# Optimization experiments

Hardware: AMD Instinct MI355X
Metric: run time of the kernel (lower is better)

Reference implementation:

```python
import jax, jax.numpy as jnp
import numpy as np

WINDOW = 5  # window_size from init
C_COARSE = 256
C_FINE = 128


def _gather_windows(fine_nchw, b, lin_idx, stride, pad, w, wc):
    """Extract [M, w*w, C] windows centered on coarse grid cells.

    Equivalent to F.unfold(kernel=w, stride=stride, padding=pad) followed by
    rearrange('n (c ww) l -> n l ww c') and fancy-indexing [b, lin_idx],
    but gathers only the matched windows.
    """
    x = jnp.pad(fine_nchw, ((0, 0), (0, 0), (pad, pad), (pad, pad)))
    x = jnp.transpose(x, (0, 2, 3, 1))  # [N, Hp, Wp, C]
    r = lin_idx // wc
    c = lin_idx % wc
    offs = jnp.arange(w)
    rows = r[:, None] * stride + offs  # [M, w] (start = r*stride - pad, +pad shift)
    cols = c[:, None] * stride + offs  # [M, w]
    patches = x[b[:, None, None], rows[:, :, None], cols[:, None, :]]  # [M, w, w, C]
    return patches.reshape(patches.shape[0], w * w, patches.shape[-1])


def setup_inputs() -> dict:
    key = jax.random.key(0)
    ks = jax.random.split(key, 10)
    N, Hc, Hf, M = 2, 60, 240, 3000
    inp = {
        "coarse_image_feature_1": jax.random.normal(ks[0], (N, Hc * Hc, C_COARSE), jnp.float32),
        "coarse_image_feature_2": jax.random.normal(ks[1], (N, Hc * Hc, C_COARSE), jnp.float32),
        "fine_image_feature_1": jax.random.normal(ks[2], (N, C_FINE, Hf, Hf), jnp.float32),
        "fine_image_feature_2": jax.random.normal(ks[3], (N, C_FINE, Hf, Hf), jnp.float32),
        "batch_indices": jax.random.randint(ks[4], (M,), 0, N),
        "row_indices": jax.random.randint(ks[5], (M,), 0, Hc * Hc),
        "column_indices": jax.random.randint(ks[6], (M,), 0, Hc * Hc),
        "fine_height_width": Hf,
        "coarse_height_width": Hc,
        # learned params (kaiming-normal-ish weights, zero biases)
        "W_dp": jax.random.normal(ks[7], (C_FINE, C_COARSE), jnp.float32) * np.sqrt(2.0 / C_FINE),
        "b_dp": jnp.zeros((C_FINE,), jnp.float32),
        "W_merge": jax.random.normal(ks[8], (C_FINE, 2 * C_FINE), jnp.float32) * np.sqrt(2.0 / C_FINE),
        "b_merge": jnp.zeros((C_FINE,), jnp.float32),
    }
    return inp


def reference(coarse_image_feature_1, coarse_image_feature_2,
              fine_image_feature_1, fine_image_feature_2,
              batch_indices, row_indices, column_indices,
              fine_height_width, coarse_height_width,
              W_dp, b_dp, W_merge, b_merge):
    stride = fine_height_width // coarse_height_width
    pad = WINDOW // 2
    M = batch_indices.shape[0]

    f1 = _gather_windows(fine_image_feature_1, batch_indices, row_indices,
                         stride, pad, WINDOW, coarse_height_width)       # [M, ww, Cf]
    f2 = _gather_windows(fine_image_feature_2, batch_indices, column_indices,
                         stride, pad, WINDOW, coarse_height_width)       # [M, ww, Cf]

    coarse = jnp.concatenate([
        coarse_image_feature_1[batch_indices, row_indices],
        coarse_image_feature_2[batch_indices, column_indices],
    ], axis=0)                                                           # [2M, Cc]
    coarse = coarse @ W_dp.T + b_dp                                      # [2M, Cf]

    fine = jnp.concatenate([f1, f2], axis=0)                             # [2M, ww, Cf]
    combined = jnp.concatenate(
        [fine, jnp.broadcast_to(coarse[:, None, :], fine.shape)], axis=-1)  # [2M, ww, 2Cf]
    merged = combined @ W_merge.T + b_merge                              # [2M, ww, Cf]
    return merged[:M], merged[M:]
```

## Files before the change

kernel.cpp:

```cpp
#include <hip/hip_runtime.h>

#define HF 240
#define HC 60
#define STRIDEF 4
#define PADW 2
#define WIN 5
#define CC 256
#define CF 128
#define NPOS 25
#define NPX (HF*HF)
#define MPB 16
#define PXT 64

typedef __bf16 bf16x8 __attribute__((ext_vector_type(8)));
typedef __bf16 bf16x4 __attribute__((ext_vector_type(4)));
typedef float  f32x4  __attribute__((ext_vector_type(4)));

__global__ void k_prep(const float* __restrict__ W_dp, const float* __restrict__ b_dp,
                       const float* __restrict__ W_merge, const float* __restrict__ b_merge,
                       __bf16* __restrict__ Wm1h, float* __restrict__ W_effT,
                       float* __restrict__ b_eff) {
    const int j = blockIdx.x;
    const int k = threadIdx.x;
    const float* wm2 = W_merge + (size_t)j * (2 * CF) + CF;

    float acc = 0.f, accb = 0.f;
    for (int q = 0; q < CF; ++q) {
        const float wq = wm2[q];
        acc  += wq * W_dp[(size_t)q * CC + k];
        accb += wq * b_dp[q];
    }
    W_effT[(size_t)k * CF + j] = acc;

    if (k < CF)
        Wm1h[(size_t)j * CF + k] = (__bf16)W_merge[(size_t)j * (2 * CF) + k];
    if (k == 0)
        b_eff[j] = accb + b_merge[j];
}

__global__ void k_coarse(const float* __restrict__ c1, const float* __restrict__ c2,
                         const int* __restrict__ bidx, const int* __restrict__ ridx,
                         const int* __restrict__ cidx, int M,
                         const float* __restrict__ W_effT, const float* __restrict__ b_eff,
                         float* __restrict__ c_all) {
    const int m0 = blockIdx.x * MPB;
    const int j  = threadIdx.x;
    const int twoM = 2 * M;
    __shared__ float v[MPB * CC];

    const int nm = (twoM - m0) < MPB ? (twoM - m0) : MPB;
    for (int mm = 0; mm < nm; ++mm) {
        int m = m0 + mm;
        const float* src;
        if (m < M) src = c1 + ((size_t)bidx[m] * (HC * HC) + ridx[m]) * CC;
        else       src = c2 + ((size_t)bidx[m - M] * (HC * HC) + cidx[m - M]) * CC;
        v[mm * CC + j]      = src[j];
        v[mm * CC + j + CF] = src[j + CF];
    }
    __syncthreads();

    float acc[MPB];
    const float be = b_eff[j];
    #pragma unroll
    for (int mm = 0; mm < MPB; ++mm) acc[mm] = be;

    for (int k = 0; k < CC; k += 4) {
        float w0 = W_effT[(k + 0) * CF + j];
        float w1 = W_effT[(k + 1) * CF + j];
        float w2 = W_effT[(k + 2) * CF + j];
        float w3 = W_effT[(k + 3) * CF + j];
        #pragma unroll
        for (int mm = 0; mm < MPB; ++mm) {
            const f32x4 vv = *(const f32x4*)&v[mm * CC + k];
            acc[mm] += w0 * vv.x + w1 * vv.y + w2 * vv.z + w3 * vv.w;
        }
    }
    for (int mm = 0; mm < nm; ++mm)
        c_all[(size_t)(m0 + mm) * CF + j] = acc[mm];
}

__global__ __launch_bounds__(256) void k_tgemm(
    const float* __restrict__ f1, const float* __restrict__ f2,
    const __bf16* __restrict__ Wm1h, __bf16* __restrict__ V) {

    const int slot = blockIdx.y;
    const float* src = (slot >= 2 ? f2 : f1) + (size_t)(slot & 1) * CF * NPX;
    const int px0 = blockIdx.x * PXT;
    const int t  = threadIdx.x;
    const int l  = t & 63;
    const int w  = t >> 6;
    const int lo16 = l & 15;
    const int hi   = l >> 4;

    __shared__ __bf16 patch[PXT * CF];

    bf16x8 bfrag[2][4];
    #pragma unroll
    for (int nt2 = 0; nt2 < 2; ++nt2) {
        const int j = w * 32 + nt2 * 16 + lo16;
        #pragma unroll
        for (int kt = 0; kt < 4; ++kt)
            bfrag[nt2][kt] = *reinterpret_cast<const bf16x8*>(Wm1h + (size_t)j * CF + kt * 32 + hi * 8);
    }

    const int pxl = 4 * lo16;
    const int sw  = lo16 << 3;
    #pragma unroll
    for (int q = 0; q < 8; ++q) {
        const int ch = w * 32 + q * 4 + hi;
        const f32x4 vv = *reinterpret_cast<const f32x4*>(src + (size_t)ch * NPX + px0 + pxl);
        const int chs = ch ^ sw;
        patch[(pxl + 0) * CF + chs] = (__bf16)vv.x;
        patch[(pxl + 1) * CF + chs] = (__bf16)vv.y;
        patch[(pxl + 2) * CF + chs] = (__bf16)vv.z;
        patch[(pxl + 3) * CF + chs] = (__bf16)vv.w;
    }
    __syncthreads();

    f32x4 acc[4][2];
    #pragma unroll
    for (int mt = 0; mt < 4; ++mt)
        #pragma unroll
        for (int nt2 = 0; nt2 < 2; ++nt2)
            acc[mt][nt2] = (f32x4){0.f, 0.f, 0.f, 0.f};

    #pragma unroll
    for (int kt = 0; kt < 4; ++kt) {
        const int k0 = kt * 32 + hi * 8;
        #pragma unroll
        for (int mt = 0; mt < 4; ++mt) {
            const int px = mt * 16 + lo16;
            const int koff = k0 ^ ((px >> 2) << 3);
            bf16x8 a = *reinterpret_cast<const bf16x8*>(&patch[px * CF + koff]);
            #pragma unroll
            for (int nt2 = 0; nt2 < 2; ++nt2)
                acc[mt][nt2] = __builtin_amdgcn_mfma_f32_16x16x32_bf16(a, bfrag[nt2][kt], acc[mt][nt2], 0, 0, 0);
        }
    }

    __bf16* Vp = V + ((size_t)slot * NPX + px0) * CF;
    #pragma unroll
    for (int mt = 0; mt < 4; ++mt) {
        #pragma unroll
        for (int nt2 = 0; nt2 < 2; ++nt2) {
            const int j = w * 32 + nt2 * 16 + lo16;
            #pragma unroll
            for (int reg = 0; reg < 4; ++reg) {
                const int px = mt * 16 + hi * 4 + reg;
                Vp[(size_t)px * CF + j] = (__bf16)acc[mt][nt2][reg];
            }
        }
    }
}

__global__ __launch_bounds__(256) void k_gather(
    const __bf16* __restrict__ V,
    const int* __restrict__ bidx, const int* __restrict__ ridx,
    const int* __restrict__ cidx, int M,
    const float* __restrict__ c_all, float* __restrict__ out) {

    const int m = blockIdx.x;
    const int t = threadIdx.x;
    const int g  = t >> 5;
    const int l32 = t & 31;

    int b, lin, ii;
    if (m < M) { ii = 0; b = bidx[m];     lin = ridx[m]; }
    else       { ii = 1; b = bidx[m - M]; lin = cidx[m - M]; }
    const int slot = ii * 2 + b;
    const int r  = lin / HC, c = lin - r * HC;
    const int y0 = r * STRIDEF - PADW;
    const int x0 = c * STRIDEF - PADW;

    const f32x4 c4 = *reinterpret_cast<const f32x4*>(c_all + (size_t)m * CF + l32 * 4);
    const __bf16* Vb = V + (size_t)slot * NPX * CF;
    float* ob = out + (size_t)m * (NPOS * CF) + l32 * 4;

    #pragma unroll
    for (int pass = 0; pass < 4; ++pass) {
        const int p = pass * 8 + g;
        if (p < NPOS) {
            const int wy = (p * 13) >> 6;
            const int wx = p - wy * WIN;
            const int y = y0 + wy, x = x0 + wx;
            f32x4 o = c4;
            if (y >= 0 && x >= 0) {
                const bf16x4 v = *reinterpret_cast<const bf16x4*>(Vb + (size_t)(y * HF + x) * CF + l32 * 4);
                o.x += (float)v.x; o.y += (float)v.y; o.z += (float)v.z; o.w += (float)v.w;
            }
            *reinterpret_cast<f32x4*>(ob + (size_t)p * CF) = o;
        }
    }
}

__global__ __launch_bounds__(256) void k_main_direct(
    const float* __restrict__ f1, const float* __restrict__ f2,
    const int* __restrict__ bidx, const int* __restrict__ ridx,
    const int* __restrict__ cidx, int M,
    const __bf16* __restrict__ Wm1h, const float* __restrict__ c_all,
    float* __restrict__ out) {

    const int m = blockIdx.x;
    const int t = threadIdx.x;
    const int l    = t & 63;
    const int wv   = t >> 6;
    const int lo16 = l & 15;
    const int hi   = l >> 4;

    __shared__ __bf16 patch[32 * CF];

    bf16x8 bfrag[2][4];
    #pragma unroll
    for (int nt2 = 0; nt2 < 2; ++nt2) {
        const int j = wv * 32 + nt2 * 16 + lo16;
        #pragma unroll
        for (int kt = 0; kt < 4; ++kt)
            bfrag[nt2][kt] = *reinterpret_cast<const bf16x8*>(Wm1h + (size_t)j * CF + kt * 32 + hi * 8);
    }

    const float* img; int b, lin;
    if (m < M) { img = f1; b = bidx[m];     lin = ridx[m]; }
    else       { img = f2; b = bidx[m - M]; lin = cidx[m - M]; }
    const int r  = lin / HC, c = lin - r * HC;
    const int y0 = r * STRIDEF - PADW;
    const int x0 = c * STRIDEF - PADW;

    for (int task = t; task < CF * WIN; task += 256) {
        const int ch = task / WIN;
        const int wy = task - ch * WIN;
        const int y  = y0 + wy;
        const bool yok = (y >= 0);
        const float* rowp = img + (((size_t)b * CF + ch) * HF + (yok ? y : 0)) * HF;
        #pragma unroll
        for (int wx = 0; wx < WIN; ++wx) {
            const int x = x0 + wx;
            const float val = (yok && x >= 0) ? rowp[x] : 0.f;
            const int pos = wy * WIN + wx;
            patch[pos * CF + (ch ^ ((pos & 7) << 3))] = (__bf16)val;
        }
    }
    __syncthreads();

    f32x4 acc[2][2];
    #pragma unroll
    for (int mt = 0; mt < 2; ++mt)
        #pragma unroll
        for (int nt2 = 0; nt2 < 2; ++nt2)
            acc[mt][nt2] = (f32x4){0.f, 0.f, 0.f, 0.f};

    const int swz = (lo16 & 7) << 3;
    #pragma unroll
    for (int kt = 0; kt < 4; ++kt) {
        const int koff = (kt * 32 + hi * 8) ^ swz;
        bf16x8 a0 = *reinterpret_cast<const bf16x8*>(&patch[ lo16       * CF + koff]);
        bf16x8 a1 = *reinterpret_cast<const bf16x8*>(&patch[(16 + lo16) * CF + koff]);
        #pragma unroll
        for (int nt2 = 0; nt2 < 2; ++nt2) {
            acc[0][nt2] = __builtin_amdgcn_mfma_f32_16x16x32_bf16(a0, bfrag[nt2][kt], acc[0][nt2], 0, 0, 0);
            acc[1][nt2] = __builtin_amdgcn_mfma_f32_16x16x32_bf16(a1, bfrag[nt2][kt], acc[1][nt2], 0, 0, 0);
        }
    }

    float* ob = out + (size_t)m * (NPOS * CF);
    #pragma unroll
    for (int nt2 = 0; nt2 < 2; ++nt2) {
        const int j  = wv * 32 + nt2 * 16 + lo16;
        const float cv = c_all[(size_t)m * CF + j];
        #pragma unroll
        for (int mt = 0; mt < 2; ++mt) {
            #pragma unroll
            for (int reg = 0; reg < 4; ++reg) {
                const int p = mt * 16 + hi * 4 + reg;
                if (p < NPOS)
                    ob[(size_t)p * CF + j] = acc[mt][nt2][reg] + cv;
            }
        }
    }
}

extern "C" void kernel_launch(void* const* d_in, const int* in_sizes, int n_in,
                              void* d_out, int out_size, void* d_ws, size_t ws_size,
                              hipStream_t stream) {
    const float* c1      = (const float*)d_in[0];
    const float* c2      = (const float*)d_in[1];
    const float* f1      = (const float*)d_in[2];
    const float* f2      = (const float*)d_in[3];
    const int*   bidx    = (const int*)d_in[4];
    const int*   ridx    = (const int*)d_in[5];
    const int*   cidx    = (const int*)d_in[6];
    const float* W_dp    = (const float*)d_in[9];
    const float* b_dp    = (const float*)d_in[10];
    const float* W_merge = (const float*)d_in[11];
    const float* b_merge = (const float*)d_in[12];
    const int M = in_sizes[4];

    char* ws = (char*)d_ws;
    __bf16* Wm1h  = (__bf16*)(ws);
    float* W_effT = (float*)(ws + (64 << 10));
    float* b_eff  = (float*)(ws + (192 << 10));
    float* c_all  = (float*)(ws + (256 << 10));
    __bf16* V     = (__bf16*)(ws + (4 << 20));

    const size_t need_V = (size_t)(4 << 20) + (size_t)4 * NPX * CF * 2;

    hipLaunchKernelGGL(k_prep, dim3(CF), dim3(CC), 0, stream,
                       W_dp, b_dp, W_merge, b_merge, Wm1h, W_effT, b_eff);
    hipLaunchKernelGGL(k_coarse, dim3((2 * M + MPB - 1) / MPB), dim3(CF), 0, stream,
                       c1, c2, bidx, ridx, cidx, M, W_effT, b_eff, c_all);

    if (ws_size >= need_V) {
        hipLaunchKernelGGL(k_tgemm, dim3(NPX / PXT, 4), dim3(256), 0, stream,
                           f1, f2, Wm1h, V);
        hipLaunchKernelGGL(k_gather, dim3(2 * M), dim3(256), 0, stream,
                           V, bidx, ridx, cidx, M, c_all, (float*)d_out);
    } else {
        hipLaunchKernelGGL(k_main_direct, dim3(2 * M), dim3(256), 0, stream,
                           f1, f2, bidx, ridx, cidx, M, Wm1h, c_all, (float*)d_out);
    }
}
```

Measured before the change: 99.45 us.

## Pipeline k_tgemm over K-chunks with double-buffered LDS and packed stores

k_tgemm now covers 128 pixels per block instead of 64 and splits the 128-channel reduction into four 32-channel chunks. It stages each chunk in a double-buffered swizzled LDS tile while the next chunk's global loads are in flight. The output column mapping is interleaved so each lane writes two adjacent bf16 values as one 32-bit store, replacing scalar bf16 writes. The intent is to overlap global loads with MFMA work, reduce LDS footprint and improve store efficiency, at the cost of more accumulator registers and extra barriers per block.

Result: faster. 95.34 us (-4.1%).

```diff
diff --git a/kernel.cpp b/kernel.cpp
--- a/kernel.cpp
+++ b/kernel.cpp
@@ -10,11 +10,14 @@
 #define NPOS 25
 #define NPX (HF*HF)
 #define MPB 16
-#define PXT 64
+#define TPX 128
+#define KCH 32
+#define NCHK 4
 
 typedef __bf16 bf16x8 __attribute__((ext_vector_type(8)));
 typedef __bf16 bf16x4 __attribute__((ext_vector_type(4)));
 typedef float  f32x4  __attribute__((ext_vector_type(4)));
+typedef float  f32x2  __attribute__((ext_vector_type(2)));
 
 __global__ void k_prep(const float* __restrict__ W_dp, const float* __restrict__ b_dp,
                        const float* __restrict__ W_merge, const float* __restrict__ b_merge,
@@ -85,72 +88,98 @@
 
     const int slot = blockIdx.y;
     const float* src = (slot >= 2 ? f2 : f1) + (size_t)(slot & 1) * CF * NPX;
-    const int px0 = blockIdx.x * PXT;
+    const int px0 = blockIdx.x * TPX;
     const int t  = threadIdx.x;
     const int l  = t & 63;
     const int w  = t >> 6;
     const int lo16 = l & 15;
     const int hi   = l >> 4;
 
-    __shared__ __bf16 patch[PXT * CF];
-
-    bf16x8 bfrag[2][4];
+    __shared__ __attribute__((aligned(16))) __bf16 chk[2][(TPX / 2) * 64];
+
+    bf16x8 bfrag[2][NCHK];
     #pragma unroll
     for (int nt2 = 0; nt2 < 2; ++nt2) {
-        const int j = w * 32 + nt2 * 16 + lo16;
-        #pragma unroll
-        for (int kt = 0; kt < 4; ++kt)
-            bfrag[nt2][kt] = *reinterpret_cast<const bf16x8*>(Wm1h + (size_t)j * CF + kt * 32 + hi * 8);
-    }
-
-    const int pxl = 4 * lo16;
-    const int sw  = lo16 << 3;
-    #pragma unroll
-    for (int q = 0; q < 8; ++q) {
-        const int ch = w * 32 + q * 4 + hi;
-        const f32x4 vv = *reinterpret_cast<const f32x4*>(src + (size_t)ch * NPX + px0 + pxl);
-        const int chs = ch ^ sw;
-        patch[(pxl + 0) * CF + chs] = (__bf16)vv.x;
-        patch[(pxl + 1) * CF + chs] = (__bf16)vv.y;
-        patch[(pxl + 2) * CF + chs] = (__bf16)vv.z;
-        patch[(pxl + 3) * CF + chs] = (__bf16)vv.w;
-    }
-    __syncthreads();
-
-    f32x4 acc[4][2];
-    #pragma unroll
-    for (int mt = 0; mt < 4; ++mt)
-        #pragma unroll
-        for (int nt2 = 0; nt2 < 2; ++nt2)
-            acc[mt][nt2] = (f32x4){0.f, 0.f, 0.f, 0.f};
-
-    #pragma unroll
-    for (int kt = 0; kt < 4; ++kt) {
-        const int k0 = kt * 32 + hi * 8;
-        #pragma unroll
-        for (int mt = 0; mt < 4; ++mt) {
+        const int j = w * 32 + 2 * lo16 + nt2;
+        #pragma unroll
+        for (int c = 0; c < NCHK; ++c)
+            bfrag[nt2][c] = *reinterpret_cast<const bf16x8*>(
+                Wm1h + (size_t)j * CF + c * KCH + hi * 8);
+    }
+
+    f32x2 vva[8], vvb[8];
+
+#define LOAD_CHUNK(c, vbuf)                                                    \
+    {                                                                          \
+        const int ch0 = (c) * KCH + w * 8;                                     \
+        _Pragma("unroll")                                                      \
+        for (int e = 0; e < 8; ++e)                                            \
+            vbuf[e] = *reinterpret_cast<const f32x2*>(                         \
+                src + (size_t)(ch0 + e) * NPX + px0 + 2 * l);                  \
+    }
+
+#define WRITE_CHUNK(buf, vbuf)                                                 \
+    {                                                                          \
+        _Pragma("unroll")                                                      \
+        for (int i = 0; i < 2; ++i) {                                          \
+            const int px = 2 * l + i;                                          \
+            bf16x8 pk;                                                         \
+            _Pragma("unroll")                                                  \
+            for (int e = 0; e < 8; ++e) pk[e] = (__bf16)vbuf[e][i];            \
+            const int rp = px >> 1;                                  \
+            const int S  = (w * 2 + (px & 1)) ^ (rp & 7);                      \
+            *reinterpret_cast<bf16x8*>(&chk[buf][rp * 64 + S * 8]) = pk;       \
+        }                                                                      \
+    }
+
+    f32x4 acc[8][2];
+    #pragma unroll
+    for (int mt = 0; mt < 8; ++mt) {
+        acc[mt][0] = (f32x4){0.f, 0.f, 0.f, 0.f};
+        acc[mt][1] = (f32x4){0.f, 0.f, 0.f, 0.f};
+    }
+
+    LOAD_CHUNK(0, vva);
+
+    #pragma unroll
+    for (int c = 0; c < NCHK; ++c) {
+        const int buf = c & 1;
+        if (buf == 0) {
+            if (c + 1 < NCHK) LOAD_CHUNK(c + 1, vvb);
+            WRITE_CHUNK(0, vva);
+        } else {
+            if (c + 1 < NCHK) LOAD_CHUNK(c + 1, vva);
+            WRITE_CHUNK(1, vvb);
+        }
+        __syncthreads();
+
+        #pragma unroll
+        for (int mt = 0; mt < 8; ++mt) {
             const int px = mt * 16 + lo16;
-            const int koff = k0 ^ ((px >> 2) << 3);
-            bf16x8 a = *reinterpret_cast<const bf16x8*>(&patch[px * CF + koff]);
-            #pragma unroll
-            for (int nt2 = 0; nt2 < 2; ++nt2)
-                acc[mt][nt2] = __builtin_amdgcn_mfma_f32_16x16x32_bf16(a, bfrag[nt2][kt], acc[mt][nt2], 0, 0, 0);
-        }
-    }
-
-    __bf16* Vp = V + ((size_t)slot * NPX + px0) * CF;
-    #pragma unroll
-    for (int mt = 0; mt < 4; ++mt) {
-        #pragma unroll
-        for (int nt2 = 0; nt2 < 2; ++nt2) {
-            const int j = w * 32 + nt2 * 16 + lo16;
-            #pragma unroll
-            for (int reg = 0; reg < 4; ++reg) {
-                const int px = mt * 16 + hi * 4 + reg;
-                Vp[(size_t)px * CF + j] = (__bf16)acc[mt][nt2][reg];
-            }
-        }
-    }
+            const int rp = px >> 1;
+            const int S  = (hi * 2 + (px & 1)) ^ (rp & 7);
+            const bf16x8 a = *reinterpret_cast<const bf16x8*>(&chk[buf][rp * 64 + S * 8]);
+            acc[mt][0] = __builtin_amdgcn_mfma_f32_16x16x32_bf16(a, bfrag[0][c], acc[mt][0], 0, 0, 0);
+            acc[mt][1] = __builtin_amdgcn_mfma_f32_16x16x32_bf16(a, bfrag[1][c], acc[mt][1], 0, 0, 0);
+        }
+        __syncthreads();
+    }
+
+    uint* Vp = (uint*)(V + ((size_t)slot * NPX + px0) * CF);
+    const int dcol = w * 16 + lo16;
+    #pragma unroll
+    for (int mt = 0; mt < 8; ++mt) {
+        #pragma unroll
+        for (int reg = 0; reg < 4; ++reg) {
+            const int px = mt * 16 + hi * 4 + reg;
+            union { uint u; __bf16 h[2]; } cv;
+            cv.h[0] = (__bf16)acc[mt][0][reg];
+            cv.h[1] = (__bf16)acc[mt][1][reg];
+            Vp[(size_t)px * 64 + dcol] = cv.u;
+        }
+    }
+#undef LOAD_CHUNK
+#undef WRITE_CHUNK
 }
 
 __global__ __launch_bounds__(256) void k_gather(
@@ -309,7 +338,7 @@
                        c1, c2, bidx, ridx, cidx, M, W_effT, b_eff, c_all);
 
     if (ws_size >= need_V) {
-        hipLaunchKernelGGL(k_tgemm, dim3(NPX / PXT, 4), dim3(256), 0, stream,
+        hipLaunchKernelGGL(k_tgemm, dim3(NPX / TPX, 4), dim3(256), 0, stream,
                            f1, f2, Wm1h, V);
         hipLaunchKernelGGL(k_gather, dim3(2 * M), dim3(256), 0, stream,
                            V, bidx, ridx, cidx, M, c_all, (float*)d_out);
```

## Restructure tgemm into 256-pixel slabs with double-buffered K-chunk pipeline

Applied to the files above, without the earlier changes.

The full-image transform GEMM now has each 512-thread block handle 256 pixels instead of 64. The channel dimension is split into four 32-wide chunks that are double-buffered in shared memory, so global loads of later chunks overlap MFMA work on earlier ones. Block indices are remapped so that each XCD processes a contiguous range of slabs. Output is written as packed pairs of bf16 values to improve store coalescing. The cost is more synchronization points, higher register pressure from the 4x4 accumulator tile, and B fragments reloaded from global memory for every chunk.

Measured after the change: 112.9 us. 13.5% more time.

```diff
diff --git a/kernel.cpp b/kernel.cpp
--- a/kernel.cpp
+++ b/kernel.cpp
@@ -10,7 +10,7 @@
 #define NPOS 25
 #define NPX (HF*HF)
 #define MPB 16
-#define PXT 64
+#define SLABS 225
 
 typedef __bf16 bf16x8 __attribute__((ext_vector_type(8)));
 typedef __bf16 bf16x4 __attribute__((ext_vector_type(4)));
@@ -79,76 +79,112 @@
         c_all[(size_t)(m0 + mm) * CF + j] = acc[mm];
 }
 
-__global__ __launch_bounds__(256) void k_tgemm(
+__global__ __launch_bounds__(512, 4) void k_tgemm(
     const float* __restrict__ f1, const float* __restrict__ f2,
     const __bf16* __restrict__ Wm1h, __bf16* __restrict__ V) {
 
+    int slab = blockIdx.x;
     const int slot = blockIdx.y;
+    {
+        const int q = SLABS / 8, r = SLABS % 8;
+        const int xcd = slab & 7, off = slab >> 3;
+        slab = (xcd < r ? xcd * (q + 1) : r * (q + 1) + (xcd - r) * q) + off;
+    }
     const float* src = (slot >= 2 ? f2 : f1) + (size_t)(slot & 1) * CF * NPX;
-    const int px0 = blockIdx.x * PXT;
-    const int t  = threadIdx.x;
-    const int l  = t & 63;
-    const int w  = t >> 6;
+    const int px0 = slab * 256;
+
+    const int t = threadIdx.x;
+    const int l = t & 63;
+    const int w = t >> 6;
     const int lo16 = l & 15;
     const int hi   = l >> 4;
-
-    __shared__ __bf16 patch[PXT * CF];
-
-    bf16x8 bfrag[2][4];
-    #pragma unroll
-    for (int nt2 = 0; nt2 < 2; ++nt2) {
-        const int j = w * 32 + nt2 * 16 + lo16;
-        #pragma unroll
-        for (int kt = 0; kt < 4; ++kt)
-            bfrag[nt2][kt] = *reinterpret_cast<const bf16x8*>(Wm1h + (size_t)j * CF + kt * 32 + hi * 8);
-    }
-
-    const int pxl = 4 * lo16;
-    const int sw  = lo16 << 3;
-    #pragma unroll
-    for (int q = 0; q < 8; ++q) {
-        const int ch = w * 32 + q * 4 + hi;
-        const f32x4 vv = *reinterpret_cast<const f32x4*>(src + (size_t)ch * NPX + px0 + pxl);
-        const int chs = ch ^ sw;
-        patch[(pxl + 0) * CF + chs] = (__bf16)vv.x;
-        patch[(pxl + 1) * CF + chs] = (__bf16)vv.y;
-        patch[(pxl + 2) * CF + chs] = (__bf16)vv.z;
-        patch[(pxl + 3) * CF + chs] = (__bf16)vv.w;
-    }
-    __syncthreads();
-
-    f32x4 acc[4][2];
+    const int mg = w >> 1;
+    const int ng = w & 1;
+
+    __shared__ __attribute__((aligned(16))) __bf16 chk[2][256 * 32];
+
+    f32x4 va[4], vb[4];
+    f32x4 acc[4][4];
     #pragma unroll
     for (int mt = 0; mt < 4; ++mt)
         #pragma unroll
-        for (int nt2 = 0; nt2 < 2; ++nt2)
-            acc[mt][nt2] = (f32x4){0.f, 0.f, 0.f, 0.f};
-
-    #pragma unroll
-    for (int kt = 0; kt < 4; ++kt) {
-        const int k0 = kt * 32 + hi * 8;
-        #pragma unroll
-        for (int mt = 0; mt < 4; ++mt) {
-            const int px = mt * 16 + lo16;
-            const int koff = k0 ^ ((px >> 2) << 3);
-            bf16x8 a = *reinterpret_cast<const bf16x8*>(&patch[px * CF + koff]);
-            #pragma unroll
-            for (int nt2 = 0; nt2 < 2; ++nt2)
-                acc[mt][nt2] = __builtin_amdgcn_mfma_f32_16x16x32_bf16(a, bfrag[nt2][kt], acc[mt][nt2], 0, 0, 0);
-        }
-    }
-
-    __bf16* Vp = V + ((size_t)slot * NPX + px0) * CF;
+        for (int nt = 0; nt < 4; ++nt)
+            acc[mt][nt] = (f32x4){0.f, 0.f, 0.f, 0.f};
+
+#define LOADC(c, vbuf)                                                        \
+    {                                                                         \
+        const int chb = (c) * 32 + w * 4;                                     \
+        _Pragma("unroll")                                                     \
+        for (int e = 0; e < 4; ++e)                                           \
+            vbuf[e] = *reinterpret_cast<const f32x4*>(                        \
+                src + (size_t)(chb + e) * NPX + px0 + 4 * l);                 \
+    }
+
+#define WRITEC(buf, vbuf)                                                     \
+    {                                                                         \
+        _Pragma("unroll")                                                     \
+        for (int i = 0; i < 4; ++i) {                                         \
+            const int px = 4 * l + i;                                         \
+            bf16x4 pk;                                                        \
+            pk[0] = (__bf16)vbuf[0][i]; pk[1] = (__bf16)vbuf[1][i];           \
+            pk[2] = (__bf16)vbuf[2][i]; pk[3] = (__bf16)vbuf[3][i];           \
+            const int g = w ^ (l & 7);                                        \
+            *reinterpret_cast<bf16x4*>(&chk[buf][px * 32 + g * 4]) = pk;      \
+        }                                                                     \
+    }
+
+#define MFMAC(c, buf)                                                         \
+    {                                                                         \
+        bf16x8 bf_[4];                                                        \
+        _Pragma("unroll")                                                     \
+        for (int nt = 0; nt < 4; ++nt) {                                      \
+            const int j = ng * 64 + (nt >> 1) * 32 + 2 * lo16 + (nt & 1);     \
+            bf_[nt] = *reinterpret_cast<const bf16x8*>(                       \
+                Wm1h + (size_t)j * CF + (c) * 32 + hi * 8);                   \
+        }                                                                     \
+        _Pragma("unroll")                                                     \
+        for (int mt = 0; mt < 4; ++mt) {                                      \
+            const int px = mg * 64 + mt * 16 + lo16;                          \
+            const int s  = (mt * 4 + (lo16 >> 2)) & 7;                        \
+            const bf16x4 a0 = *reinterpret_cast<const bf16x4*>(               \
+                &chk[buf][px * 32 + (((2 * hi) ^ s) << 2)]);                  \
+            const bf16x4 a1 = *reinterpret_cast<const bf16x4*>(               \
+                &chk[buf][px * 32 + (((2 * hi + 1) ^ s) << 2)]);              \
+            bf16x8 a;                                                         \
+            a[0] = a0[0]; a[1] = a0[1]; a[2] = a0[2]; a[3] = a0[3];           \
+            a[4] = a1[0]; a[5] = a1[1]; a[6] = a1[2]; a[7] = a1[3];           \
+            _Pragma("unroll")                                                 \
+            for (int nt = 0; nt < 4; ++nt)                                    \
+                acc[mt][nt] = __builtin_amdgcn_mfma_f32_16x16x32_bf16(        \
+                    a, bf_[nt], acc[mt][nt], 0, 0, 0);                        \
+        }                                                                     \
+    }
+
+    LOADC(0, va);
+    LOADC(1, vb);
+    WRITEC(0, va);
+    __syncthreads();  LOADC(2, va);  WRITEC(1, vb);  MFMAC(0, 0);
+    __syncthreads();  LOADC(3, vb);  WRITEC(0, va);  MFMAC(1, 1);
+    __syncthreads();                 WRITEC(1, vb);  MFMAC(2, 0);
+    __syncthreads();                                 MFMAC(3, 1);
+
+#undef LOADC
+#undef WRITEC
+#undef MFMAC
+
+    uint* Vp = (uint*)(V + ((size_t)slot * NPX + px0) * CF);
     #pragma unroll
     for (int mt = 0; mt < 4; ++mt) {
         #pragma unroll
-        for (int nt2 = 0; nt2 < 2; ++nt2) {
-            const int j = w * 32 + nt2 * 16 + lo16;
-            #pragma unroll
-            for (int reg = 0; reg < 4; ++reg) {
-                const int px = mt * 16 + hi * 4 + reg;
-                Vp[(size_t)px * CF + j] = (__bf16)acc[mt][nt2][reg];
-            }
+        for (int reg = 0; reg < 4; ++reg) {
+            const int px = mg * 64 + mt * 16 + hi * 4 + reg;
+            union { uint u; __bf16 h[2]; } cv;
+            cv.h[0] = (__bf16)acc[mt][0][reg];
+            cv.h[1] = (__bf16)acc[mt][1][reg];
+            Vp[(size_t)px * 64 + ng * 32 + lo16] = cv.u;
+            cv.h[0] = (__bf16)acc[mt][2][reg];
+            cv.h[1] = (__bf16)acc[mt][3][reg];
+            Vp[(size_t)px * 64 + ng * 32 + 16 + lo16] = cv.u;
         }
     }
 }
@@ -309,7 +345,7 @@
                        c1, c2, bidx, ridx, cidx, M, W_effT, b_eff, c_all);
 
     if (ws_size >= need_V) {
-        hipLaunchKernelGGL(k_tgemm, dim3(NPX / PXT, 4), dim3(256), 0, stream,
+        hipLaunchKernelGGL(k_tgemm, dim3(SLABS, 4), dim3(512), 0, stream,
                            f1, f2, Wm1h, V);
         hipLaunchKernelGGL(k_gather, dim3(2 * M), dim3(256), 0, stream,
                            V, bidx, ridx, cidx, M, c_all, (float*)d_out);
```
